# Optimization experiments

Measured on AMD Instinct MI355X. Metric: run time of the kernel, lower is better.

The kernel has to match this reference:

```python
import jax, jax.numpy as jnp
import numpy as np

EPS = 1e-8


def setup_inputs() -> dict:
    key = jax.random.key(0)
    k1, k2, k3, k4 = jax.random.split(key, 4)
    B, S, H, D, E = 2, 2048, 1024, 4096, 8
    x = jax.random.normal(k1, (B, S, H), dtype=jnp.float32)
    routing_weights = jax.random.uniform(k2, (B, S, E), dtype=jnp.float32)
    # xavier-uniform-like scale for the expert weight tensors
    lim_d = float(np.sqrt(6.0 / (H + D)))
    lim_u = float(np.sqrt(6.0 / (D + H)))
    down_weights = jax.random.uniform(k3, (E, H, D), dtype=jnp.float32, minval=-lim_d, maxval=lim_d)
    up_weights = jax.random.uniform(k4, (E, D, H), dtype=jnp.float32, minval=-lim_u, maxval=lim_u)
    down_biases = jnp.zeros((E, D), dtype=jnp.float32)
    return {
        "x": x,
        "routing_weights": routing_weights,
        "down_weights": down_weights,
        "down_biases": down_biases,
        "up_weights": up_weights,
        "top_k": 2,
    }


def reference(x, routing_weights, down_weights, down_biases, up_weights, top_k):
    """SmearExpert.forward with routing_strategy='top_k_sparse' (3D routing weights).
    Returns (output, sparse_weights) exactly as the torch module does."""
    B, S, H = x.shape
    E = down_weights.shape[0]

    # top-k sparsification + renormalization of the routing weights
    topk_w, topk_i = jax.lax.top_k(routing_weights, top_k)          # [B,S,k]
    sparse_w = (jax.nn.one_hot(topk_i, E, dtype=x.dtype) * topk_w[..., None]).sum(-2)  # [B,S,E]
    sparse_w = sparse_w / (sparse_w.sum(-1, keepdims=True) + EPS)

    x_flat = x.reshape(-1, H)              # [T,H]
    w_flat = sparse_w.reshape(-1, E)       # [T,E]

    # per-expert down-proj -> GELU(exact) -> up-proj, combined with routing weights
    # (tokens with zero weight contribute nothing, matching the masked torch path)
    out = jnp.zeros_like(x_flat)
    for e in range(E):
        z = jax.nn.gelu(x_flat @ down_weights[e] + down_biases[e], approximate=False)  # [T,D]
        out = out + (z @ up_weights[e]) * w_flat[:, e:e + 1]
    return out.reshape(B, S, H), sparse_w
```

## Files before the change

### kernel.cpp

```cpp
#include <hip/hip_runtime.h>
#include <stdint.h>

#define T_TOK 4096
#define HDIM  1024
#define DDIM  4096
#define NEXP  8

typedef unsigned short ushort_t;
typedef __attribute__((ext_vector_type(8))) short bf16x8;
typedef __attribute__((ext_vector_type(4))) float f32x4;

__device__ __forceinline__ float bf2f(ushort_t b) {
  return __uint_as_float(((unsigned int)b) << 16);
}
__device__ __forceinline__ unsigned int f2bf(float f) {
  unsigned int u = __float_as_uint(f);
  return (u + 0x7fffu + ((u >> 16) & 1u)) >> 16;
}

__device__ __forceinline__ void gld16(const void* g, void* l) {
  __builtin_amdgcn_global_load_lds(
      (const __attribute__((address_space(1))) unsigned int*)g,
      (__attribute__((address_space(3))) unsigned int*)l, 16, 0, 0);
}

__global__ void k_init(int* counts) {
  if (threadIdx.x < NEXP) counts[threadIdx.x] = 0;
}

__global__ void k_route(const float* __restrict__ rw, float* __restrict__ sw_out,
                        int* counts, int* inv_e, int* inv_p, float* inv_w,
                        int* tokA) {
  int t = blockIdx.x * 256 + threadIdx.x;
  if (t >= T_TOK) return;
  float v[NEXP];
#pragma unroll
  for (int e = 0; e < NEXP; e++) v[e] = rw[t * NEXP + e];
  int i0 = 0; float m0 = v[0];
#pragma unroll
  for (int e = 1; e < NEXP; e++) if (v[e] > m0) { m0 = v[e]; i0 = e; }
  int i1 = -1; float m1 = -1e30f;
#pragma unroll
  for (int e = 0; e < NEXP; e++) if (e != i0 && v[e] > m1) { m1 = v[e]; i1 = e; }
  float s = m0 + m1 + 1e-8f;
  float w0 = m0 / s, w1 = m1 / s;
#pragma unroll
  for (int e = 0; e < NEXP; e++) {
    float w = (e == i0) ? w0 : ((e == i1) ? w1 : 0.0f);
    sw_out[t * NEXP + e] = w;
  }
  int p0 = atomicAdd(&counts[i0], 1);
  int p1 = atomicAdd(&counts[i1], 1);
  tokA[i0 * T_TOK + p0] = t;
  tokA[i1 * T_TOK + p1] = t;
  inv_e[t * 2] = i0; inv_e[t * 2 + 1] = i1;
  inv_p[t * 2] = p0; inv_p[t * 2 + 1] = p1;
  inv_w[t * 2] = w0; inv_w[t * 2 + 1] = w1;
}

__global__ void k_offsets(const int* counts, int* offsets) {
  int acc = 0;
  for (int e = 0; e < NEXP; e++) { offsets[e] = acc; acc += counts[e]; }
}

__global__ __launch_bounds__(256)
void k_cvtx(const float* __restrict__ x, ushort_t* __restrict__ xb) {
  size_t i = (size_t)blockIdx.x * 256 + threadIdx.x;
  float4 f0 = ((const float4*)x)[i * 2];
  float4 f1 = ((const float4*)x)[i * 2 + 1];
  uint4 o;
  o.x = f2bf(f0.x) | (f2bf(f0.y) << 16);
  o.y = f2bf(f0.z) | (f2bf(f0.w) << 16);
  o.z = f2bf(f1.x) | (f2bf(f1.y) << 16);
  o.w = f2bf(f1.z) | (f2bf(f1.w) << 16);
  ((uint4*)xb)[i] = o;
}

template <int KDIM, int NDIM>
__global__ __launch_bounds__(256)
void k_cvtw(const float* __restrict__ W, ushort_t* __restrict__ Wt) {
  constexpr int KT = KDIM / 64;
  __shared__ __align__(16) short sh[128 * 64];
  const int ekt = blockIdx.y;
  const int e  = ekt / KT;
  const int kt = ekt % KT;
  const int n0 = blockIdx.x * 128;
  const int tid = threadIdx.x;
  const int t_d = tid & 15;
  const int t_k = tid >> 4;
  const float* bp = W + (size_t)e * KDIM * NDIM + (size_t)(kt * 64 + t_k * 4) * NDIM + n0 + t_d * 8;
  float r0[8], r1[8], r2[8], r3[8];
  *(float4*)(r0)     = ((const float4*)(bp))[0];
  *(float4*)(r0 + 4) = ((const float4*)(bp))[1];
  *(float4*)(r1)     = ((const float4*)(bp + NDIM))[0];
  *(float4*)(r1 + 4) = ((const float4*)(bp + NDIM))[1];
  *(float4*)(r2)     = ((const float4*)(bp + 2 * NDIM))[0];
  *(float4*)(r2 + 4) = ((const float4*)(bp + 2 * NDIM))[1];
  *(float4*)(r3)     = ((const float4*)(bp + 3 * NDIM))[0];
  *(float4*)(r3 + 4) = ((const float4*)(bp + 3 * NDIM))[1];
#pragma unroll
  for (int j = 0; j < 8; j++) {
    int jj = j ^ (t_d & 7);
    int nl = t_d * 8 + jj;
    int cs = (t_k >> 1) ^ jj;
    uint2 wv;
    wv.x = f2bf(r0[jj]) | (f2bf(r1[jj]) << 16);
    wv.y = f2bf(r2[jj]) | (f2bf(r3[jj]) << 16);
    *(uint2*)(sh + nl * 64 + cs * 8 + (t_k & 1) * 4) = wv;
  }
  __syncthreads();
  ushort_t* outp = Wt + ((size_t)ekt * NDIM + n0) * 64;
#pragma unroll
  for (int it = 0; it < 4; ++it) {
    size_t off = (size_t)it * 4096 + tid * 16;
    *(uint4*)((char*)outp + off) = *(const uint4*)((const char*)sh + off);
  }
}

template <int KDIM, int NDIM, bool DOWN>
__global__ __launch_bounds__(256, 3)
void k_gemm(const ushort_t* __restrict__ Asrc, const ushort_t* __restrict__ Wt,
            const float* __restrict__ bias, const int* __restrict__ counts,
            const int* __restrict__ offsets, const int* __restrict__ tokA,
            ushort_t* __restrict__ Out) {
  constexpr int KT = KDIM / 64;
  __shared__ __align__(16) short a_sh[128 * 64];
  __shared__ __align__(16) short b_sh[128 * 64];
  const int e    = blockIdx.y >> 5;
  const int tile = blockIdx.y & 31;
  const int cnt  = counts[e];
  if (tile * 128 >= cnt) return;
  const int off_e = offsets[e];
  const int zbase = off_e + tile * 128;
  const int n0    = blockIdx.x * 128;
  const int tid   = threadIdx.x;
  const int wave  = tid >> 6;
  const int lane  = tid & 63;
  const int rgrp  = lane >> 3;
  const int lc    = lane & 7;

  const ushort_t* abase[4];
#pragma unroll
  for (int i = 0; i < 4; i++) {
    int rl = wave * 32 + i * 8 + rgrp;
    int ridx = tile * 128 + rl;
    int ridx_c = (ridx < cnt) ? ridx : tile * 128;
    size_t row;
    if constexpr (DOWN) row = (size_t)tokA[e * T_TOK + ridx_c];
    else                row = (size_t)(off_e + ridx_c);
    abase[i] = Asrc + row * KDIM + ((lc ^ (rl & 7)) * 8);
  }
  const ushort_t* bbase = Wt + ((size_t)e * KT * NDIM + n0) * 64 + wave * 2048 + lane * 8;
  char* a_seg = (char*)a_sh + wave * 4096;
  char* b_seg = (char*)b_sh + wave * 4096;

  const int lm   = lane & 15;
  const int quad = lane >> 4;

  f32x4 acc[8][2];
  const f32x4 zero = {0.0f, 0.0f, 0.0f, 0.0f};
#pragma unroll
  for (int mf = 0; mf < 8; mf++)
#pragma unroll
    for (int nf = 0; nf < 2; nf++) acc[mf][nf] = zero;

  for (int kt = 0; kt < KT; ++kt) {
#pragma unroll
    for (int it = 0; it < 4; ++it)
      gld16(abase[it] + kt * 64, a_seg + it * 1024);
    const ushort_t* bg = bbase + (size_t)kt * (NDIM * 64);
#pragma unroll
    for (int it = 0; it < 4; ++it)
      gld16(bg + it * 512, b_seg + it * 1024);
    __syncthreads();
#pragma unroll
    for (int ks = 0; ks < 2; ++ks) {
      bf16x8 af[8];
#pragma unroll
      for (int mf = 0; mf < 8; mf++) {
        int m = mf * 16 + lm;
        int cc = (ks * 4 + quad) ^ (lm & 7);
        af[mf] = *(const bf16x8*)(a_sh + m * 64 + cc * 8);
      }
      bf16x8 bfv[2];
#pragma unroll
      for (int nf = 0; nf < 2; nf++) {
        int n = wave * 32 + nf * 16 + lm;
        int cc = (ks * 4 + quad) ^ (lm & 7);
        bfv[nf] = *(const bf16x8*)(b_sh + n * 64 + cc * 8);
      }
#pragma unroll
      for (int mf = 0; mf < 8; mf++)
#pragma unroll
        for (int nf = 0; nf < 2; nf++)
          acc[mf][nf] = __builtin_amdgcn_mfma_f32_16x16x32_bf16(af[mf], bfv[nf], acc[mf][nf], 0, 0, 0);
    }
    __syncthreads();
  }

  float bv[2] = {0.0f, 0.0f};
  if constexpr (DOWN) {
#pragma unroll
    for (int nf = 0; nf < 2; nf++)
      bv[nf] = bias[e * NDIM + n0 + wave * 32 + nf * 16 + lm];
  }
  short* ep = ((wave & 2) ? b_sh : a_sh) + (wave & 1) * 4096;
#pragma unroll
  for (int mf = 0; mf < 8; mf++)
#pragma unroll
    for (int nf = 0; nf < 2; nf++)
#pragma unroll
      for (int r = 0; r < 4; r++) {
        float v = acc[mf][nf][r];
        if constexpr (DOWN) {
          float zv = v + bv[nf];
          v = 0.5f * zv * (1.0f + erff(zv * 0.70710678118654752f));
        }
        ep[(mf * 16 + quad * 4 + r) * 32 + nf * 16 + lm] = (short)f2bf(v);
      }
  __syncthreads();
#pragma unroll
  for (int it = 0; it < 8; ++it) {
    int row = it * 16 + (lane >> 2);
    uint4 v = *(const uint4*)(ep + row * 32 + (lane & 3) * 8);
    if (tile * 128 + row < cnt)
      *(uint4*)(Out + (size_t)(zbase + row) * NDIM + n0 + wave * 32 + (lane & 3) * 8) = v;
  }
}

__global__ void k_combine(const ushort_t* __restrict__ U, const int* __restrict__ inv_e,
                          const int* __restrict__ inv_p, const float* __restrict__ inv_w,
                          const int* __restrict__ offsets, float* __restrict__ out) {
  int gid = blockIdx.x * 256 + threadIdx.x;
  int t  = gid >> 7;
  int hc = (gid & 127) * 8;
  int e0 = inv_e[t * 2], e1 = inv_e[t * 2 + 1];
  size_t s0 = (size_t)offsets[e0] + inv_p[t * 2];
  size_t s1 = (size_t)offsets[e1] + inv_p[t * 2 + 1];
  float w0 = inv_w[t * 2], w1 = inv_w[t * 2 + 1];
  const ushort_t* u0 = U + s0 * HDIM + hc;
  const ushort_t* u1 = U + s1 * HDIM + hc;
  uint4 q0 = *(const uint4*)u0;
  uint4 q1 = *(const uint4*)u1;
  const ushort_t* a = (const ushort_t*)&q0;
  const ushort_t* b = (const ushort_t*)&q1;
  float4 o0, o1;
  o0.x = w0 * bf2f(a[0]) + w1 * bf2f(b[0]);
  o0.y = w0 * bf2f(a[1]) + w1 * bf2f(b[1]);
  o0.z = w0 * bf2f(a[2]) + w1 * bf2f(b[2]);
  o0.w = w0 * bf2f(a[3]) + w1 * bf2f(b[3]);
  o1.x = w0 * bf2f(a[4]) + w1 * bf2f(b[4]);
  o1.y = w0 * bf2f(a[5]) + w1 * bf2f(b[5]);
  o1.z = w0 * bf2f(a[6]) + w1 * bf2f(b[6]);
  o1.w = w0 * bf2f(a[7]) + w1 * bf2f(b[7]);
  float* op = out + (size_t)t * HDIM + hc;
  *(float4*)(op)     = o0;
  *(float4*)(op + 4) = o1;
}

extern "C" void kernel_launch(void* const* d_in, const int* in_sizes, int n_in,
                              void* d_out, int out_size, void* d_ws, size_t ws_size,
                              hipStream_t stream) {
  const float* x  = (const float*)d_in[0];
  const float* rw = (const float*)d_in[1];
  const float* wd = (const float*)d_in[2];
  const float* bd = (const float*)d_in[3];
  const float* wu = (const float*)d_in[4];
  float* out    = (float*)d_out;
  float* sw_out = out + (size_t)T_TOK * HDIM;

  char* ws = (char*)d_ws;
  int*      counts = (int*)(ws);
  int*      offs   = (int*)(ws + 64);
  int*      inv_e  = (int*)(ws + 128);
  int*      inv_p  = (int*)(ws + 128 + 32768);
  float*    inv_w  = (float*)(ws + 128 + 65536);
  int*      tokA   = (int*)(ws + 128 + 98304);
  size_t    base   = 262144;
  ushort_t* Z      = (ushort_t*)(ws + base);
  ushort_t* U      = (ushort_t*)(ws + base + 67108864);
  ushort_t* xbf    = (ushort_t*)(ws + base + 67108864 + 16777216);
  ushort_t* Wt     = (ushort_t*)(ws + base + 67108864 + 16777216 + 8388608);

  k_init<<<1, 64, 0, stream>>>(counts);
  k_route<<<T_TOK / 256, 256, 0, stream>>>(rw, sw_out, counts, inv_e, inv_p, inv_w, tokA);
  k_offsets<<<1, 1, 0, stream>>>(counts, offs);
  k_cvtx<<<T_TOK * HDIM / 8 / 256, 256, 0, stream>>>(x, xbf);
  k_cvtw<HDIM, DDIM><<<dim3(DDIM / 128, NEXP * (HDIM / 64)), 256, 0, stream>>>(wd, Wt);
  k_gemm<HDIM, DDIM, true><<<dim3(DDIM / 128, NEXP * 32), 256, 0, stream>>>(
      xbf, Wt, bd, counts, offs, tokA, Z);
  k_cvtw<DDIM, HDIM><<<dim3(HDIM / 128, NEXP * (DDIM / 64)), 256, 0, stream>>>(wu, Wt);
  k_gemm<DDIM, HDIM, false><<<dim3(HDIM / 128, NEXP * 32), 256, 0, stream>>>(
      Z, Wt, nullptr, counts, offs, tokA, U);
  k_combine<<<(T_TOK * HDIM / 8) / 256, 256, 0, stream>>>(U, inv_e, inv_p, inv_w, offs, out);
}
```

Before: 683.7 us.

## Double-buffer GEMM LDS tiles and simplify weight-conversion kernel without LDS

The expert GEMM now keeps two LDS buffers for the A and B tiles and issues the async global-to-LDS loads for the next K-step while MFMAs run on the current one. This is meant to hide global load latency behind compute. The doubled LDS footprint lowers the occupancy hint from 3 to 2 blocks per CU. The fp32-to-bf16 weight transpose kernel is also rewritten so each thread converts one output column, with no shared-memory staging. Its writes become 16-byte stores at a 128-byte stride across threads.

```diff
diff --git a/kernel.cpp b/kernel.cpp
--- a/kernel.cpp
+++ b/kernel.cpp
@@ -80,52 +80,41 @@
 __global__ __launch_bounds__(256)
 void k_cvtw(const float* __restrict__ W, ushort_t* __restrict__ Wt) {
   constexpr int KT = KDIM / 64;
-  __shared__ __align__(16) short sh[128 * 64];
   const int ekt = blockIdx.y;
   const int e  = ekt / KT;
   const int kt = ekt % KT;
-  const int n0 = blockIdx.x * 128;
-  const int tid = threadIdx.x;
-  const int t_d = tid & 15;
-  const int t_k = tid >> 4;
-  const float* bp = W + (size_t)e * KDIM * NDIM + (size_t)(kt * 64 + t_k * 4) * NDIM + n0 + t_d * 8;
-  float r0[8], r1[8], r2[8], r3[8];
-  *(float4*)(r0)     = ((const float4*)(bp))[0];
-  *(float4*)(r0 + 4) = ((const float4*)(bp))[1];
-  *(float4*)(r1)     = ((const float4*)(bp + NDIM))[0];
-  *(float4*)(r1 + 4) = ((const float4*)(bp + NDIM))[1];
-  *(float4*)(r2)     = ((const float4*)(bp + 2 * NDIM))[0];
-  *(float4*)(r2 + 4) = ((const float4*)(bp + 2 * NDIM))[1];
-  *(float4*)(r3)     = ((const float4*)(bp + 3 * NDIM))[0];
-  *(float4*)(r3 + 4) = ((const float4*)(bp + 3 * NDIM))[1];
-#pragma unroll
-  for (int j = 0; j < 8; j++) {
-    int jj = j ^ (t_d & 7);
-    int nl = t_d * 8 + jj;
-    int cs = (t_k >> 1) ^ jj;
-    uint2 wv;
-    wv.x = f2bf(r0[jj]) | (f2bf(r1[jj]) << 16);
-    wv.y = f2bf(r2[jj]) | (f2bf(r3[jj]) << 16);
-    *(uint2*)(sh + nl * 64 + cs * 8 + (t_k & 1) * 4) = wv;
-  }
-  __syncthreads();
-  ushort_t* outp = Wt + ((size_t)ekt * NDIM + n0) * 64;
-#pragma unroll
-  for (int it = 0; it < 4; ++it) {
-    size_t off = (size_t)it * 4096 + tid * 16;
-    *(uint4*)((char*)outp + off) = *(const uint4*)((const char*)sh + off);
+  const int n  = blockIdx.x * 256 + threadIdx.x;
+  const float* src = W + (size_t)e * KDIM * NDIM + (size_t)(kt * 64) * NDIM + n;
+  ushort_t* dst = Wt + ((size_t)ekt * NDIM + n) * 64;
+  const int sw = n & 7;
+#pragma unroll
+  for (int g = 0; g < 8; ++g) {
+    float v0 = src[(size_t)(g * 8 + 0) * NDIM];
+    float v1 = src[(size_t)(g * 8 + 1) * NDIM];
+    float v2 = src[(size_t)(g * 8 + 2) * NDIM];
+    float v3 = src[(size_t)(g * 8 + 3) * NDIM];
+    float v4 = src[(size_t)(g * 8 + 4) * NDIM];
+    float v5 = src[(size_t)(g * 8 + 5) * NDIM];
+    float v6 = src[(size_t)(g * 8 + 6) * NDIM];
+    float v7 = src[(size_t)(g * 8 + 7) * NDIM];
+    uint4 o;
+    o.x = f2bf(v0) | (f2bf(v1) << 16);
+    o.y = f2bf(v2) | (f2bf(v3) << 16);
+    o.z = f2bf(v4) | (f2bf(v5) << 16);
+    o.w = f2bf(v6) | (f2bf(v7) << 16);
+    *(uint4*)(dst + (g ^ sw) * 8) = o;
   }
 }
 
 template <int KDIM, int NDIM, bool DOWN>
-__global__ __launch_bounds__(256, 3)
+__global__ __launch_bounds__(256, 2)
 void k_gemm(const ushort_t* __restrict__ Asrc, const ushort_t* __restrict__ Wt,
             const float* __restrict__ bias, const int* __restrict__ counts,
             const int* __restrict__ offsets, const int* __restrict__ tokA,
             ushort_t* __restrict__ Out) {
   constexpr int KT = KDIM / 64;
-  __shared__ __align__(16) short a_sh[128 * 64];
-  __shared__ __align__(16) short b_sh[128 * 64];
+  __shared__ __align__(16) short a_sh[2][128 * 64];
+  __shared__ __align__(16) short b_sh[2][128 * 64];
   const int e    = blockIdx.y >> 5;
   const int tile = blockIdx.y & 31;
   const int cnt  = counts[e];
@@ -151,8 +140,6 @@
     abase[i] = Asrc + row * KDIM + ((lc ^ (rl & 7)) * 8);
   }
   const ushort_t* bbase = Wt + ((size_t)e * KT * NDIM + n0) * 64 + wave * 2048 + lane * 8;
-  char* a_seg = (char*)a_sh + wave * 4096;
-  char* b_seg = (char*)b_sh + wave * 4096;
 
   const int lm   = lane & 15;
   const int quad = lane >> 4;
@@ -164,7 +151,9 @@
 #pragma unroll
     for (int nf = 0; nf < 2; nf++) acc[mf][nf] = zero;
 
-  for (int kt = 0; kt < KT; ++kt) {
+  auto stage = [&](int buf, int kt) {
+    char* a_seg = (char*)a_sh[buf] + wave * 4096;
+    char* b_seg = (char*)b_sh[buf] + wave * 4096;
 #pragma unroll
     for (int it = 0; it < 4; ++it)
       gld16(abase[it] + kt * 64, a_seg + it * 1024);
@@ -172,7 +161,16 @@
 #pragma unroll
     for (int it = 0; it < 4; ++it)
       gld16(bg + it * 512, b_seg + it * 1024);
-    __syncthreads();
+  };
+
+  stage(0, 0);
+  __syncthreads();
+
+  for (int kt = 0; kt < KT; ++kt) {
+    const int cur = kt & 1;
+    if (kt + 1 < KT) stage(cur ^ 1, kt + 1);
+    const short* ab = a_sh[cur];
+    const short* bb = b_sh[cur];
 #pragma unroll
     for (int ks = 0; ks < 2; ++ks) {
       bf16x8 af[8];
@@ -180,14 +178,14 @@
       for (int mf = 0; mf < 8; mf++) {
         int m = mf * 16 + lm;
         int cc = (ks * 4 + quad) ^ (lm & 7);
-        af[mf] = *(const bf16x8*)(a_sh + m * 64 + cc * 8);
+        af[mf] = *(const bf16x8*)(ab + m * 64 + cc * 8);
       }
       bf16x8 bfv[2];
 #pragma unroll
       for (int nf = 0; nf < 2; nf++) {
         int n = wave * 32 + nf * 16 + lm;
         int cc = (ks * 4 + quad) ^ (lm & 7);
-        bfv[nf] = *(const bf16x8*)(b_sh + n * 64 + cc * 8);
+        bfv[nf] = *(const bf16x8*)(bb + n * 64 + cc * 8);
       }
 #pragma unroll
       for (int mf = 0; mf < 8; mf++)
@@ -204,7 +202,7 @@
     for (int nf = 0; nf < 2; nf++)
       bv[nf] = bias[e * NDIM + n0 + wave * 32 + nf * 16 + lm];
   }
-  short* ep = ((wave & 2) ? b_sh : a_sh) + (wave & 1) * 4096;
+  short* ep = (short*)a_sh + wave * 4096;
 #pragma unroll
   for (int mf = 0; mf < 8; mf++)
 #pragma unroll
@@ -286,10 +284,10 @@
   k_route<<<T_TOK / 256, 256, 0, stream>>>(rw, sw_out, counts, inv_e, inv_p, inv_w, tokA);
   k_offsets<<<1, 1, 0, stream>>>(counts, offs);
   k_cvtx<<<T_TOK * HDIM / 8 / 256, 256, 0, stream>>>(x, xbf);
-  k_cvtw<HDIM, DDIM><<<dim3(DDIM / 128, NEXP * (HDIM / 64)), 256, 0, stream>>>(wd, Wt);
+  k_cvtw<HDIM, DDIM><<<dim3(DDIM / 256, NEXP * (HDIM / 64)), 256, 0, stream>>>(wd, Wt);
   k_gemm<HDIM, DDIM, true><<<dim3(DDIM / 128, NEXP * 32), 256, 0, stream>>>(
       xbf, Wt, bd, counts, offs, tokA, Z);
-  k_cvtw<DDIM, HDIM><<<dim3(HDIM / 128, NEXP * (DDIM / 64)), 256, 0, stream>>>(wu, Wt);
+  k_cvtw<DDIM, HDIM><<<dim3(HDIM / 256, NEXP * (DDIM / 64)), 256, 0, stream>>>(wu, Wt);
   k_gemm<DDIM, HDIM, false><<<dim3(HDIM / 128, NEXP * 32), 256, 0, stream>>>(
       Z, Wt, nullptr, counts, offs, tokA, U);
   k_combine<<<(T_TOK * HDIM / 8) / 256, 256, 0, stream>>>(U, inv_e, inv_p, inv_w, offs, out);
```

Result: slower. 727.4 us (+6.4%).
